# Performance work log

Measured on AMD Instinct MI355X. Metric: run time of the kernel, lower is better.

Reference implementation:

```python
import jax, jax.numpy as jnp
import numpy as np

NODE_DIM = 128
EDGE_DIM = 128
N_NODES = 10000
N_EDGES = 640000


def setup_inputs() -> dict:
    key = jax.random.key(0)
    ks = jax.random.split(key, 11)
    x = jax.random.normal(ks[0], (N_NODES, NODE_DIM), dtype=jnp.float32)
    edge_index = jax.random.randint(ks[1], (2, N_EDGES), 0, N_NODES, dtype=jnp.int32)
    edge_attr = jax.random.normal(ks[2], (N_EDGES, EDGE_DIM), dtype=jnp.float32)

    def lin(k, fan_in, fan_out):
        kw, kb = jax.random.split(k)
        bound = 1.0 / np.sqrt(fan_in)
        W = jax.random.uniform(kw, (fan_in, fan_out), minval=-bound, maxval=bound, dtype=jnp.float32)
        b = jax.random.uniform(kb, (fan_out,), minval=-bound, maxval=bound, dtype=jnp.float32)
        return W, b

    # node_update: Linear(node+edge -> node), Softplus, Linear(node -> node)
    nW1, nb1 = lin(ks[3], NODE_DIM + EDGE_DIM, NODE_DIM)
    nW2, nb2 = lin(ks[4], NODE_DIM, NODE_DIM)
    # edge_update_net: Linear(2*node+edge -> edge), Softplus, Linear(edge -> edge)
    eW1, eb1 = lin(ks[5], 2 * NODE_DIM + EDGE_DIM, EDGE_DIM)
    eW2, eb2 = lin(ks[6], EDGE_DIM, EDGE_DIM)

    return {
        "x": x, "edge_index": edge_index, "edge_attr": edge_attr,
        "nW1": nW1, "nb1": nb1, "nW2": nW2, "nb2": nb2,
        "eW1": eW1, "eb1": eb1, "eW2": eW2, "eb2": eb2,
    }


def reference(x, edge_index, edge_attr, nW1, nb1, nW2, nb2, eW1, eb1, eW2, eb2):
    row, col = edge_index[0], edge_index[1]
    x_row = x[row]              # [E, node_dim]
    x_col = x[col]              # [E, node_dim]

    # edge update MLP
    edge_input = jnp.concatenate([x_row, x_col, edge_attr], axis=1)  # [E, 2n+e]
    h = jax.nn.softplus(edge_input @ eW1 + eb1)
    edge_attr_new = h @ eW2 + eb2                                     # [E, edge_dim]

    # node message MLP
    msg_in = jnp.concatenate([x_row, edge_attr_new], axis=1)          # [E, n+e]
    m = jax.nn.softplus(msg_in @ nW1 + nb1)
    messages = m @ nW2 + nb2                                          # [E, node_dim]

    # scatter_add messages into destination nodes (col)
    x_new = jax.ops.segment_sum(messages, col, num_segments=x.shape[0])
    return (x_new, edge_attr_new)
```

## Files before the change

### kernel.cpp

```cpp
#include <hip/hip_runtime.h>
#include <cstdint>

#define N_NODES   10000
#define N_EDGES   640000
#define NODE_OUT  (N_NODES * 128)

typedef __bf16 bf16;
typedef bf16  bf16x8 __attribute__((ext_vector_type(8)));
typedef float f32x4  __attribute__((ext_vector_type(4)));

#define EW1T_OFF 0
#define EW2T_OFF 49152
#define NW1T_OFF 65536
#define NW2T_OFF 98304

__global__ void transpose_weights(const float* __restrict__ eW1, const float* __restrict__ eW2,
                                  const float* __restrict__ nW1, const float* __restrict__ nW2,
                                  bf16* __restrict__ wt) {
  int gid = blockIdx.x * 256 + threadIdx.x;
  const float* src; bf16* dst; int K, off;
  if (gid < 49152)      { src = eW1; dst = wt + EW1T_OFF; K = 384; off = gid; }
  else if (gid < 65536) { src = eW2; dst = wt + EW2T_OFF; K = 128; off = gid - 49152; }
  else if (gid < 98304) { src = nW1; dst = wt + NW1T_OFF; K = 256; off = gid - 65536; }
  else                  { src = nW2; dst = wt + NW2T_OFF; K = 128; off = gid - 98304; }
  int k = off >> 7, n = off & 127;
  dst[n * K + k] = (bf16)src[off];
}

__device__ __forceinline__ float softplus_f(float v) {
  return v > 20.f ? v : __logf(1.f + __expf(v));
}

__device__ __forceinline__ bf16x8 load_cvt8(const float* __restrict__ src) {
  float4 f0 = *(const float4*)src;
  float4 f1 = *(const float4*)(src + 4);
  bf16x8 h;
  h[0] = (bf16)f0.x; h[1] = (bf16)f0.y; h[2] = (bf16)f0.z; h[3] = (bf16)f0.w;
  h[4] = (bf16)f1.x; h[5] = (bf16)f1.y; h[6] = (bf16)f1.z; h[7] = (bf16)f1.w;
  return h;
}

__global__ void __launch_bounds__(256, 2)
edge_mlp(const float* __restrict__ x, const int* __restrict__ eidx,
         const float* __restrict__ edge_attr,
         const float* __restrict__ eb1, const float* __restrict__ eb2,
         const bf16* __restrict__ wt,
         float* __restrict__ edge_out)
{
  __shared__ bf16 sA[64 * 384];
  __shared__ bf16 sC[64 * 128];

  const int tid  = threadIdx.x;
  const int wave = tid >> 6, lane = tid & 63;
  const int ln15 = lane & 15, lq = lane >> 4;
  const int n0 = wave * 32;
  const int sw = ln15 & 7;

  bf16x8 w1[12][2], w2[4][2];
  #pragma unroll
  for (int c = 0; c < 12; ++c)
    #pragma unroll
    for (int t = 0; t < 2; ++t)
      w1[c][t] = *(const bf16x8*)&wt[EW1T_OFF + (n0 + t * 16 + ln15) * 384 + c * 32 + lq * 8];
  #pragma unroll
  for (int c = 0; c < 4; ++c)
    #pragma unroll
    for (int t = 0; t < 2; ++t)
      w2[c][t] = *(const bf16x8*)&wt[EW2T_OFF + (n0 + t * 16 + ln15) * 128 + c * 32 + lq * 8];
  float b1[2], b2[2];
  #pragma unroll
  for (int t = 0; t < 2; ++t) {
    b1[t] = eb1[n0 + t * 16 + ln15];
    b2[t] = eb2[n0 + t * 16 + ln15];
  }

  for (int tile = blockIdx.x; tile < N_EDGES / 64; tile += gridDim.x) {
    const int e0 = tile * 64;

    #pragma unroll
    for (int it = 0; it < 12; ++it) {
      int j  = it * 256 + tid;
      int region = j >> 10;
      int jj = j & 1023;
      int e  = jj >> 4, pl = jj & 15;
      int lp = pl ^ (e & 7);
      const float* src;
      if (region == 0)      src = x + (size_t)eidx[e0 + e] * 128 + lp * 8;
      else if (region == 1) src = x + (size_t)eidx[N_EDGES + e0 + e] * 128 + lp * 8;
      else                  src = edge_attr + (size_t)(e0 + e) * 128 + lp * 8;
      *(bf16x8*)&sA[e * 384 + ((region << 4) + pl) * 8] = load_cvt8(src);
    }
    __syncthreads();

    f32x4 acc[4][2];
    #pragma unroll
    for (int mf = 0; mf < 4; ++mf)
      #pragma unroll
      for (int t = 0; t < 2; ++t)
        acc[mf][t] = f32x4{0.f, 0.f, 0.f, 0.f};
    #pragma unroll
    for (int c = 0; c < 12; ++c) {
      bf16x8 a[4];
      #pragma unroll
      for (int mf = 0; mf < 4; ++mf)
        a[mf] = *(const bf16x8*)&sA[(mf * 16 + ln15) * 384 + ((((c << 2) + lq) ^ sw) << 3)];
      #pragma unroll
      for (int mf = 0; mf < 4; ++mf)
        #pragma unroll
        for (int t = 0; t < 2; ++t)
          acc[mf][t] = __builtin_amdgcn_mfma_f32_16x16x32_bf16(a[mf], w1[c][t], acc[mf][t], 0, 0, 0);
    }

    #pragma unroll
    for (int mf = 0; mf < 4; ++mf)
      #pragma unroll
      for (int t = 0; t < 2; ++t)
        #pragma unroll
        for (int r = 0; r < 4; ++r) {
          float v = softplus_f(acc[mf][t][r] + b1[t]);
          int row = mf * 16 + lq * 4 + r;
          int col = n0 + t * 16 + ln15;
          int ls  = col >> 3;
          sC[row * 128 + ((ls ^ (row & 7)) << 3) + (col & 7)] = (bf16)v;
        }
    __syncthreads();

    #pragma unroll
    for (int mf = 0; mf < 4; ++mf)
      #pragma unroll
      for (int t = 0; t < 2; ++t)
        acc[mf][t] = f32x4{0.f, 0.f, 0.f, 0.f};
    #pragma unroll
    for (int c = 0; c < 4; ++c) {
      bf16x8 a[4];
      #pragma unroll
      for (int mf = 0; mf < 4; ++mf)
        a[mf] = *(const bf16x8*)&sC[(mf * 16 + ln15) * 128 + ((((c << 2) + lq) ^ sw) << 3)];
      #pragma unroll
      for (int mf = 0; mf < 4; ++mf)
        #pragma unroll
        for (int t = 0; t < 2; ++t)
          acc[mf][t] = __builtin_amdgcn_mfma_f32_16x16x32_bf16(a[mf], w2[c][t], acc[mf][t], 0, 0, 0);
    }
    #pragma unroll
    for (int mf = 0; mf < 4; ++mf)
      #pragma unroll
      for (int t = 0; t < 2; ++t)
        #pragma unroll
        for (int r = 0; r < 4; ++r) {
          int row = mf * 16 + lq * 4 + r;
          int col = n0 + t * 16 + ln15;
          edge_out[(size_t)(e0 + row) * 128 + col] = acc[mf][t][r] + b2[t];
        }
  }
}

__global__ void __launch_bounds__(256, 2)
node_mlp(const float* __restrict__ x, const int* __restrict__ eidx,
         const float* __restrict__ edge_new,
         const float* __restrict__ nb1, const float* __restrict__ nb2,
         const bf16* __restrict__ wt,
         float* __restrict__ node_out)
{
  __shared__ bf16 sA[64 * 384];

  const int tid  = threadIdx.x;
  const int wave = tid >> 6, lane = tid & 63;
  const int ln15 = lane & 15, lq = lane >> 4;
  const int n0 = wave * 32;
  const int sw = ln15 & 7;

  bf16x8 w3[8][2], w4[4][2];
  #pragma unroll
  for (int c = 0; c < 8; ++c)
    #pragma unroll
    for (int t = 0; t < 2; ++t)
      w3[c][t] = *(const bf16x8*)&wt[NW1T_OFF + (n0 + t * 16 + ln15) * 256 + c * 32 + lq * 8];
  #pragma unroll
  for (int c = 0; c < 4; ++c)
    #pragma unroll
    for (int t = 0; t < 2; ++t)
      w4[c][t] = *(const bf16x8*)&wt[NW2T_OFF + (n0 + t * 16 + ln15) * 128 + c * 32 + lq * 8];
  float b3[2], b4[2];
  #pragma unroll
  for (int t = 0; t < 2; ++t) {
    b3[t] = nb1[n0 + t * 16 + ln15];
    b4[t] = nb2[n0 + t * 16 + ln15];
  }

  for (int tile = blockIdx.x; tile < N_EDGES / 64; tile += gridDim.x) {
    const int e0 = tile * 64;

    #pragma unroll
    for (int it = 0; it < 8; ++it) {
      int j  = it * 256 + tid;
      int region = j >> 10;
      int jj = j & 1023;
      int e  = jj >> 4, pl = jj & 15;
      int lp = pl ^ (e & 7);
      const float* src = (region == 0)
          ? x + (size_t)eidx[e0 + e] * 128 + lp * 8
          : edge_new + (size_t)(e0 + e) * 128 + lp * 8;
      *(bf16x8*)&sA[e * 384 + ((region << 4) + pl) * 8] = load_cvt8(src);
    }
    __syncthreads();

    f32x4 acc[4][2];
    #pragma unroll
    for (int mf = 0; mf < 4; ++mf)
      #pragma unroll
      for (int t = 0; t < 2; ++t)
        acc[mf][t] = f32x4{0.f, 0.f, 0.f, 0.f};
    #pragma unroll
    for (int c = 0; c < 8; ++c) {
      bf16x8 a[4];
      #pragma unroll
      for (int mf = 0; mf < 4; ++mf)
        a[mf] = *(const bf16x8*)&sA[(mf * 16 + ln15) * 384 + ((((c << 2) + lq) ^ sw) << 3)];
      #pragma unroll
      for (int mf = 0; mf < 4; ++mf)
        #pragma unroll
        for (int t = 0; t < 2; ++t)
          acc[mf][t] = __builtin_amdgcn_mfma_f32_16x16x32_bf16(a[mf], w3[c][t], acc[mf][t], 0, 0, 0);
    }

    #pragma unroll
    for (int mf = 0; mf < 4; ++mf)
      #pragma unroll
      for (int t = 0; t < 2; ++t)
        #pragma unroll
        for (int r = 0; r < 4; ++r) {
          float v = softplus_f(acc[mf][t][r] + b3[t]);
          int row = mf * 16 + lq * 4 + r;
          int col = n0 + t * 16 + ln15;
          int ls  = 32 + (col >> 3);
          sA[row * 384 + ((ls ^ (row & 7)) << 3) + (col & 7)] = (bf16)v;
        }
    __syncthreads();

    #pragma unroll
    for (int mf = 0; mf < 4; ++mf)
      #pragma unroll
      for (int t = 0; t < 2; ++t)
        acc[mf][t] = f32x4{0.f, 0.f, 0.f, 0.f};
    #pragma unroll
    for (int c = 0; c < 4; ++c) {
      bf16x8 a[4];
      #pragma unroll
      for (int mf = 0; mf < 4; ++mf)
        a[mf] = *(const bf16x8*)&sA[(mf * 16 + ln15) * 384 + (((32 + (c << 2) + lq) ^ sw) << 3)];
      #pragma unroll
      for (int mf = 0; mf < 4; ++mf)
        #pragma unroll
        for (int t = 0; t < 2; ++t)
          acc[mf][t] = __builtin_amdgcn_mfma_f32_16x16x32_bf16(a[mf], w4[c][t], acc[mf][t], 0, 0, 0);
    }
    #pragma unroll
    for (int mf = 0; mf < 4; ++mf) {
      int nodes[4];
      #pragma unroll
      for (int r = 0; r < 4; ++r)
        nodes[r] = eidx[N_EDGES + e0 + mf * 16 + lq * 4 + r];
      #pragma unroll
      for (int t = 0; t < 2; ++t) {
        int col = n0 + t * 16 + ln15;
        #pragma unroll
        for (int r = 0; r < 4; ++r) {
          float v = acc[mf][t][r] + b4[t];
          unsafeAtomicAdd(&node_out[(size_t)nodes[r] * 128 + col], v);
        }
      }
    }
  }
}

extern "C" void kernel_launch(void* const* d_in, const int* in_sizes, int n_in,
                              void* d_out, int out_size, void* d_ws, size_t ws_size,
                              hipStream_t stream) {
  const float* x    = (const float*)d_in[0];
  const int*   eidx = (const int*)d_in[1];
  const float* ea   = (const float*)d_in[2];
  const float* nW1  = (const float*)d_in[3];
  const float* nb1  = (const float*)d_in[4];
  const float* nW2  = (const float*)d_in[5];
  const float* nb2  = (const float*)d_in[6];
  const float* eW1  = (const float*)d_in[7];
  const float* eb1  = (const float*)d_in[8];
  const float* eW2  = (const float*)d_in[9];
  const float* eb2  = (const float*)d_in[10];

  bf16*  wt        = (bf16*)d_ws;
  float* out_nodes = (float*)d_out;
  float* out_edges = out_nodes + NODE_OUT;

  hipMemsetAsync(out_nodes, 0, NODE_OUT * sizeof(float), stream);
  transpose_weights<<<448, 256, 0, stream>>>(eW1, eW2, nW1, nW2, wt);
  edge_mlp<<<512, 256, 0, stream>>>(x, eidx, ea, eb1, eb2, wt, out_edges);
  node_mlp<<<512, 256, 0, stream>>>(x, eidx, out_edges, nb1, nb2, wt, out_nodes);
}
```

Baseline: 992.5 us.

## Prefetch next edge tile into registers, halve tile size, and pre-convert x to bf16

Edge and node MLP kernels now use 32-edge tiles and software-pipeline the gathers: the next tile's x rows and edge features are loaded into registers while the current tile is computed. When workspace allows, x is converted to bf16 once so gathers read half the bytes. The smaller tile roughly halves LDS use, which may raise occupancy, but it also halves MFMA work per barrier and adds register pressure from the prefetch buffers.

New measurement: 839.2 us. 1.18x faster.

```diff
diff --git a/kernel.cpp b/kernel.cpp
--- a/kernel.cpp
+++ b/kernel.cpp
@@ -13,6 +13,8 @@
 #define EW2T_OFF 49152
 #define NW1T_OFF 65536
 #define NW2T_OFF 98304
+#define XB_OFF   114688
+#define WS_NEED_BYTES (229376 + 2560000)
 
 __global__ void transpose_weights(const float* __restrict__ eW1, const float* __restrict__ eW2,
                                   const float* __restrict__ nW1, const float* __restrict__ nW2,
@@ -31,24 +33,33 @@
   return v > 20.f ? v : __logf(1.f + __expf(v));
 }
 
-__device__ __forceinline__ bf16x8 load_cvt8(const float* __restrict__ src) {
-  float4 f0 = *(const float4*)src;
-  float4 f1 = *(const float4*)(src + 4);
+__device__ __forceinline__ bf16x8 cvt8(float4 f0, float4 f1) {
   bf16x8 h;
   h[0] = (bf16)f0.x; h[1] = (bf16)f0.y; h[2] = (bf16)f0.z; h[3] = (bf16)f0.w;
   h[4] = (bf16)f1.x; h[5] = (bf16)f1.y; h[6] = (bf16)f1.z; h[7] = (bf16)f1.w;
   return h;
 }
 
+__device__ __forceinline__ bf16x8 load_cvt8(const float* __restrict__ src) {
+  float4 f0 = *(const float4*)src;
+  float4 f1 = *(const float4*)(src + 4);
+  return cvt8(f0, f1);
+}
+
+__global__ void convert_x(const float* __restrict__ x, bf16* __restrict__ xb) {
+  int i = (blockIdx.x * 256 + threadIdx.x) * 8;
+  *(bf16x8*)&xb[i] = load_cvt8(x + i);
+}
+
+template<bool XB>
 __global__ void __launch_bounds__(256, 2)
-edge_mlp(const float* __restrict__ x, const int* __restrict__ eidx,
-         const float* __restrict__ edge_attr,
+edge_mlp(const float* __restrict__ x, const bf16* __restrict__ xb,
+         const int* __restrict__ eidx, const float* __restrict__ edge_attr,
          const float* __restrict__ eb1, const float* __restrict__ eb2,
-         const bf16* __restrict__ wt,
-         float* __restrict__ edge_out)
+         const bf16* __restrict__ wt, float* __restrict__ edge_out)
 {
-  __shared__ bf16 sA[64 * 384];
-  __shared__ bf16 sC[64 * 128];
+  __shared__ bf16 sA[32 * 384];
+  __shared__ bf16 sC[32 * 128];
 
   const int tid  = threadIdx.x;
   const int wave = tid >> 6, lane = tid & 63;
@@ -74,45 +85,104 @@
     b2[t] = eb2[n0 + t * 16 + ln15];
   }
 
-  for (int tile = blockIdx.x; tile < N_EDGES / 64; tile += gridDim.x) {
-    const int e0 = tile * 64;
-
-    #pragma unroll
-    for (int it = 0; it < 12; ++it) {
-      int j  = it * 256 + tid;
-      int region = j >> 10;
-      int jj = j & 1023;
-      int e  = jj >> 4, pl = jj & 15;
-      int lp = pl ^ (e & 7);
-      const float* src;
-      if (region == 0)      src = x + (size_t)eidx[e0 + e] * 128 + lp * 8;
-      else if (region == 1) src = x + (size_t)eidx[N_EDGES + e0 + e] * 128 + lp * 8;
-      else                  src = edge_attr + (size_t)(e0 + e) * 128 + lp * 8;
-      *(bf16x8*)&sA[e * 384 + ((region << 4) + pl) * 8] = load_cvt8(src);
+  const int eA = tid >> 4, eB = eA + 16;
+  const int pl = tid & 15, lp = pl ^ (eA & 7);
+
+  uint4  hx0, hx1, hc0, hc1;
+  float4 px0[2], px1[2], pc0[2], pc1[2];
+  float4 pa0[2], pa1[2];
+
+  const int NT = N_EDGES / 32;
+
+  {
+    const int e0 = blockIdx.x * 32;
+    int riA = eidx[e0 + eA], riB = eidx[e0 + eB];
+    int ciA = eidx[N_EDGES + e0 + eA], ciB = eidx[N_EDGES + e0 + eB];
+    if constexpr (XB) {
+      hx0 = *(const uint4*)&xb[(size_t)riA * 128 + lp * 8];
+      hx1 = *(const uint4*)&xb[(size_t)riB * 128 + lp * 8];
+      hc0 = *(const uint4*)&xb[(size_t)ciA * 128 + lp * 8];
+      hc1 = *(const uint4*)&xb[(size_t)ciB * 128 + lp * 8];
+    } else {
+      px0[0] = *(const float4*)(x + (size_t)riA * 128 + lp * 8);
+      px0[1] = *(const float4*)(x + (size_t)riA * 128 + lp * 8 + 4);
+      px1[0] = *(const float4*)(x + (size_t)riB * 128 + lp * 8);
+      px1[1] = *(const float4*)(x + (size_t)riB * 128 + lp * 8 + 4);
+      pc0[0] = *(const float4*)(x + (size_t)ciA * 128 + lp * 8);
+      pc0[1] = *(const float4*)(x + (size_t)ciA * 128 + lp * 8 + 4);
+      pc1[0] = *(const float4*)(x + (size_t)ciB * 128 + lp * 8);
+      pc1[1] = *(const float4*)(x + (size_t)ciB * 128 + lp * 8 + 4);
+    }
+    pa0[0] = *(const float4*)(edge_attr + (size_t)(e0 + eA) * 128 + lp * 8);
+    pa0[1] = *(const float4*)(edge_attr + (size_t)(e0 + eA) * 128 + lp * 8 + 4);
+    pa1[0] = *(const float4*)(edge_attr + (size_t)(e0 + eB) * 128 + lp * 8);
+    pa1[1] = *(const float4*)(edge_attr + (size_t)(e0 + eB) * 128 + lp * 8 + 4);
+  }
+
+  for (int tile = blockIdx.x; tile < NT; tile += gridDim.x) {
+    const int e0 = tile * 32;
+
+    if constexpr (XB) {
+      *(uint4*)&sA[eA * 384 + (0 * 16 + pl) * 8] = hx0;
+      *(uint4*)&sA[eB * 384 + (0 * 16 + pl) * 8] = hx1;
+      *(uint4*)&sA[eA * 384 + (1 * 16 + pl) * 8] = hc0;
+      *(uint4*)&sA[eB * 384 + (1 * 16 + pl) * 8] = hc1;
+    } else {
+      *(bf16x8*)&sA[eA * 384 + (0 * 16 + pl) * 8] = cvt8(px0[0], px0[1]);
+      *(bf16x8*)&sA[eB * 384 + (0 * 16 + pl) * 8] = cvt8(px1[0], px1[1]);
+      *(bf16x8*)&sA[eA * 384 + (1 * 16 + pl) * 8] = cvt8(pc0[0], pc0[1]);
+      *(bf16x8*)&sA[eB * 384 + (1 * 16 + pl) * 8] = cvt8(pc1[0], pc1[1]);
+    }
+    *(bf16x8*)&sA[eA * 384 + (2 * 16 + pl) * 8] = cvt8(pa0[0], pa0[1]);
+    *(bf16x8*)&sA[eB * 384 + (2 * 16 + pl) * 8] = cvt8(pa1[0], pa1[1]);
+
+    const int tn = tile + gridDim.x;
+    if (tn < NT) {
+      const int en = tn * 32;
+      int riA = eidx[en + eA], riB = eidx[en + eB];
+      int ciA = eidx[N_EDGES + en + eA], ciB = eidx[N_EDGES + en + eB];
+      if constexpr (XB) {
+        hx0 = *(const uint4*)&xb[(size_t)riA * 128 + lp * 8];
+        hx1 = *(const uint4*)&xb[(size_t)riB * 128 + lp * 8];
+        hc0 = *(const uint4*)&xb[(size_t)ciA * 128 + lp * 8];
+        hc1 = *(const uint4*)&xb[(size_t)ciB * 128 + lp * 8];
+      } else {
+        px0[0] = *(const float4*)(x + (size_t)riA * 128 + lp * 8);
+        px0[1] = *(const float4*)(x + (size_t)riA * 128 + lp * 8 + 4);
+        px1[0] = *(const float4*)(x + (size_t)riB * 128 + lp * 8);
+        px1[1] = *(const float4*)(x + (size_t)riB * 128 + lp * 8 + 4);
+        pc0[0] = *(const float4*)(x + (size_t)ciA * 128 + lp * 8);
+        pc0[1] = *(const float4*)(x + (size_t)ciA * 128 + lp * 8 + 4);
+        pc1[0] = *(const float4*)(x + (size_t)ciB * 128 + lp * 8);
+        pc1[1] = *(const float4*)(x + (size_t)ciB * 128 + lp * 8 + 4);
+      }
+      pa0[0] = *(const float4*)(edge_attr + (size_t)(en + eA) * 128 + lp * 8);
+      pa0[1] = *(const float4*)(edge_attr + (size_t)(en + eA) * 128 + lp * 8 + 4);
+      pa1[0] = *(const float4*)(edge_attr + (size_t)(en + eB) * 128 + lp * 8);
+      pa1[1] = *(const float4*)(edge_attr + (size_t)(en + eB) * 128 + lp * 8 + 4);
     }
     __syncthreads();
 
-    f32x4 acc[4][2];
-    #pragma unroll
-    for (int mf = 0; mf < 4; ++mf)
+    f32x4 acc[2][2];
+    #pragma unroll
+    for (int mf = 0; mf < 2; ++mf)
       #pragma unroll
       for (int t = 0; t < 2; ++t)
         acc[mf][t] = f32x4{0.f, 0.f, 0.f, 0.f};
     #pragma unroll
     for (int c = 0; c < 12; ++c) {
-      bf16x8 a[4];
-      #pragma unroll
-      for (int mf = 0; mf < 4; ++mf)
-        a[mf] = *(const bf16x8*)&sA[(mf * 16 + ln15) * 384 + ((((c << 2) + lq) ^ sw) << 3)];
-      #pragma unroll
-      for (int mf = 0; mf < 4; ++mf)
-        #pragma unroll
-        for (int t = 0; t < 2; ++t)
-          acc[mf][t] = __builtin_amdgcn_mfma_f32_16x16x32_bf16(a[mf], w1[c][t], acc[mf][t], 0, 0, 0);
-    }
-
-    #pragma unroll
-    for (int mf = 0; mf < 4; ++mf)
+      int s = (((c * 4 + lq) ^ sw) << 3);
+      bf16x8 a0 = *(const bf16x8*)&sA[ln15 * 384 + s];
+      bf16x8 a1 = *(const bf16x8*)&sA[(16 + ln15) * 384 + s];
+      #pragma unroll
+      for (int t = 0; t < 2; ++t) {
+        acc[0][t] = __builtin_amdgcn_mfma_f32_16x16x32_bf16(a0, w1[c][t], acc[0][t], 0, 0, 0);
+        acc[1][t] = __builtin_amdgcn_mfma_f32_16x16x32_bf16(a1, w1[c][t], acc[1][t], 0, 0, 0);
+      }
+    }
+
+    #pragma unroll
+    for (int mf = 0; mf < 2; ++mf)
       #pragma unroll
       for (int t = 0; t < 2; ++t)
         #pragma unroll
@@ -120,49 +190,47 @@
           float v = softplus_f(acc[mf][t][r] + b1[t]);
           int row = mf * 16 + lq * 4 + r;
           int col = n0 + t * 16 + ln15;
-          int ls  = col >> 3;
-          sC[row * 128 + ((ls ^ (row & 7)) << 3) + (col & 7)] = (bf16)v;
+          sC[row * 128 + ((((col >> 3) ^ (row & 7))) << 3) + (col & 7)] = (bf16)v;
         }
     __syncthreads();
 
-    #pragma unroll
-    for (int mf = 0; mf < 4; ++mf)
-      #pragma unroll
-      for (int t = 0; t < 2; ++t)
-        acc[mf][t] = f32x4{0.f, 0.f, 0.f, 0.f};
+    f32x4 d[2][2];
+    #pragma unroll
+    for (int mf = 0; mf < 2; ++mf)
+      #pragma unroll
+      for (int t = 0; t < 2; ++t)
+        d[mf][t] = f32x4{0.f, 0.f, 0.f, 0.f};
     #pragma unroll
     for (int c = 0; c < 4; ++c) {
-      bf16x8 a[4];
-      #pragma unroll
-      for (int mf = 0; mf < 4; ++mf)
-        a[mf] = *(const bf16x8*)&sC[(mf * 16 + ln15) * 128 + ((((c << 2) + lq) ^ sw) << 3)];
-      #pragma unroll
-      for (int mf = 0; mf < 4; ++mf)
-        #pragma unroll
-        for (int t = 0; t < 2; ++t)
-          acc[mf][t] = __builtin_amdgcn_mfma_f32_16x16x32_bf16(a[mf], w2[c][t], acc[mf][t], 0, 0, 0);
-    }
-    #pragma unroll
-    for (int mf = 0; mf < 4; ++mf)
+      int s = (((c * 4 + lq) ^ sw) << 3);
+      bf16x8 a0 = *(const bf16x8*)&sC[ln15 * 128 + s];
+      bf16x8 a1 = *(const bf16x8*)&sC[(16 + ln15) * 128 + s];
+      #pragma unroll
+      for (int t = 0; t < 2; ++t) {
+        d[0][t] = __builtin_amdgcn_mfma_f32_16x16x32_bf16(a0, w2[c][t], d[0][t], 0, 0, 0);
+        d[1][t] = __builtin_amdgcn_mfma_f32_16x16x32_bf16(a1, w2[c][t], d[1][t], 0, 0, 0);
+      }
+    }
+    #pragma unroll
+    for (int mf = 0; mf < 2; ++mf)
       #pragma unroll
       for (int t = 0; t < 2; ++t)
         #pragma unroll
         for (int r = 0; r < 4; ++r) {
           int row = mf * 16 + lq * 4 + r;
-          int col = n0 + t * 16 + ln15;
-          edge_out[(size_t)(e0 + row) * 128 + col] = acc[mf][t][r] + b2[t];
+          edge_out[(size_t)(e0 + row) * 128 + n0 + t * 16 + ln15] = d[mf][t][r] + b2[t];
         }
   }
 }
 
+template<bool XB>
 __global__ void __launch_bounds__(256, 2)
-node_mlp(const float* __restrict__ x, const int* __restrict__ eidx,
-         const float* __restrict__ edge_new,
+node_mlp(const float* __restrict__ x, const bf16* __restrict__ xb,
+         const int* __restrict__ eidx, const float* __restrict__ edge_new,
          const float* __restrict__ nb1, const float* __restrict__ nb2,
-         const bf16* __restrict__ wt,
-         float* __restrict__ node_out)
+         const bf16* __restrict__ wt, float* __restrict__ node_out)
 {
-  __shared__ bf16 sA[64 * 384];
+  __shared__ bf16 sA[32 * 384];
 
   const int tid  = threadIdx.x;
   const int wave = tid >> 6, lane = tid & 63;
@@ -188,44 +256,86 @@
     b4[t] = nb2[n0 + t * 16 + ln15];
   }
 
-  for (int tile = blockIdx.x; tile < N_EDGES / 64; tile += gridDim.x) {
-    const int e0 = tile * 64;
-
-    #pragma unroll
-    for (int it = 0; it < 8; ++it) {
-      int j  = it * 256 + tid;
-      int region = j >> 10;
-      int jj = j & 1023;
-      int e  = jj >> 4, pl = jj & 15;
-      int lp = pl ^ (e & 7);
-      const float* src = (region == 0)
-          ? x + (size_t)eidx[e0 + e] * 128 + lp * 8
-          : edge_new + (size_t)(e0 + e) * 128 + lp * 8;
-      *(bf16x8*)&sA[e * 384 + ((region << 4) + pl) * 8] = load_cvt8(src);
+  const int eA = tid >> 4, eB = eA + 16;
+  const int pl = tid & 15, lp = pl ^ (eA & 7);
+
+  uint4  hx0, hx1;
+  float4 px0[2], px1[2];
+  float4 pe0[2], pe1[2];
+
+  const int NT = N_EDGES / 32;
+
+  {
+    const int e0 = blockIdx.x * 32;
+    int riA = eidx[e0 + eA], riB = eidx[e0 + eB];
+    if constexpr (XB) {
+      hx0 = *(const uint4*)&xb[(size_t)riA * 128 + lp * 8];
+      hx1 = *(const uint4*)&xb[(size_t)riB * 128 + lp * 8];
+    } else {
+      px0[0] = *(const float4*)(x + (size_t)riA * 128 + lp * 8);
+      px0[1] = *(const float4*)(x + (size_t)riA * 128 + lp * 8 + 4);
+      px1[0] = *(const float4*)(x + (size_t)riB * 128 + lp * 8);
+      px1[1] = *(const float4*)(x + (size_t)riB * 128 + lp * 8 + 4);
+    }
+    pe0[0] = *(const float4*)(edge_new + (size_t)(e0 + eA) * 128 + lp * 8);
+    pe0[1] = *(const float4*)(edge_new + (size_t)(e0 + eA) * 128 + lp * 8 + 4);
+    pe1[0] = *(const float4*)(edge_new + (size_t)(e0 + eB) * 128 + lp * 8);
+    pe1[1] = *(const float4*)(edge_new + (size_t)(e0 + eB) * 128 + lp * 8 + 4);
+  }
+
+  for (int tile = blockIdx.x; tile < NT; tile += gridDim.x) {
+    const int e0 = tile * 32;
+
+    if constexpr (XB) {
+      *(uint4*)&sA[eA * 384 + (0 * 16 + pl) * 8] = hx0;
+      *(uint4*)&sA[eB * 384 + (0 * 16 + pl) * 8] = hx1;
+    } else {
+      *(bf16x8*)&sA[eA * 384 + (0 * 16 + pl) * 8] = cvt8(px0[0], px0[1]);
+      *(bf16x8*)&sA[eB * 384 + (0 * 16 + pl) * 8] = cvt8(px1[0], px1[1]);
+    }
+    *(bf16x8*)&sA[eA * 384 + (1 * 16 + pl) * 8] = cvt8(pe0[0], pe0[1]);
+    *(bf16x8*)&sA[eB * 384 + (1 * 16 + pl) * 8] = cvt8(pe1[0], pe1[1]);
+
+    const int tn = tile + gridDim.x;
+    if (tn < NT) {
+      const int en = tn * 32;
+      int riA = eidx[en + eA], riB = eidx[en + eB];
+      if constexpr (XB) {
+        hx0 = *(const uint4*)&xb[(size_t)riA * 128 + lp * 8];
+        hx1 = *(const uint4*)&xb[(size_t)riB * 128 + lp * 8];
+      } else {
+        px0[0] = *(const float4*)(x + (size_t)riA * 128 + lp * 8);
+        px0[1] = *(const float4*)(x + (size_t)riA * 128 + lp * 8 + 4);
+        px1[0] = *(const float4*)(x + (size_t)riB * 128 + lp * 8);
+        px1[1] = *(const float4*)(x + (size_t)riB * 128 + lp * 8 + 4);
+      }
+      pe0[0] = *(const float4*)(edge_new + (size_t)(en + eA) * 128 + lp * 8);
+      pe0[1] = *(const float4*)(edge_new + (size_t)(en + eA) * 128 + lp * 8 + 4);
+      pe1[0] = *(const float4*)(edge_new + (size_t)(en + eB) * 128 + lp * 8);
+      pe1[1] = *(const float4*)(edge_new + (size_t)(en + eB) * 128 + lp * 8 + 4);
     }
     __syncthreads();
 
-    f32x4 acc[4][2];
-    #pragma unroll
-    for (int mf = 0; mf < 4; ++mf)
+    f32x4 acc[2][2];
+    #pragma unroll
+    for (int mf = 0; mf < 2; ++mf)
       #pragma unroll
       for (int t = 0; t < 2; ++t)
         acc[mf][t] = f32x4{0.f, 0.f, 0.f, 0.f};
     #pragma unroll
     for (int c = 0; c < 8; ++c) {
-      bf16x8 a[4];
-      #pragma unroll
-      for (int mf = 0; mf < 4; ++mf)
-        a[mf] = *(const bf16x8*)&sA[(mf * 16 + ln15) * 384 + ((((c << 2) + lq) ^ sw) << 3)];
-      #pragma unroll
-      for (int mf = 0; mf < 4; ++mf)
-        #pragma unroll
-        for (int t = 0; t < 2; ++t)
-          acc[mf][t] = __builtin_amdgcn_mfma_f32_16x16x32_bf16(a[mf], w3[c][t], acc[mf][t], 0, 0, 0);
-    }
-
-    #pragma unroll
-    for (int mf = 0; mf < 4; ++mf)
+      int s = (((c * 4 + lq) ^ sw) << 3);
+      bf16x8 a0 = *(const bf16x8*)&sA[ln15 * 384 + s];
+      bf16x8 a1 = *(const bf16x8*)&sA[(16 + ln15) * 384 + s];
+      #pragma unroll
+      for (int t = 0; t < 2; ++t) {
+        acc[0][t] = __builtin_amdgcn_mfma_f32_16x16x32_bf16(a0, w3[c][t], acc[0][t], 0, 0, 0);
+        acc[1][t] = __builtin_amdgcn_mfma_f32_16x16x32_bf16(a1, w3[c][t], acc[1][t], 0, 0, 0);
+      }
+    }
+
+    #pragma unroll
+    for (int mf = 0; mf < 2; ++mf)
       #pragma unroll
       for (int t = 0; t < 2; ++t)
         #pragma unroll
@@ -238,36 +348,34 @@
         }
     __syncthreads();
 
-    #pragma unroll
-    for (int mf = 0; mf < 4; ++mf)
-      #pragma unroll
-      for (int t = 0; t < 2; ++t)
-        acc[mf][t] = f32x4{0.f, 0.f, 0.f, 0.f};
+    f32x4 d[2][2];
+    #pragma unroll
+    for (int mf = 0; mf < 2; ++mf)
+      #pragma unroll
+      for (int t = 0; t < 2; ++t)
+        d[mf][t] = f32x4{0.f, 0.f, 0.f, 0.f};
     #pragma unroll
     for (int c = 0; c < 4; ++c) {
-      bf16x8 a[4];
-      #pragma unroll
-      for (int mf = 0; mf < 4; ++mf)
-        a[mf] = *(const bf16x8*)&sA[(mf * 16 + ln15) * 384 + (((32 + (c << 2) + lq) ^ sw) << 3)];
-      #pragma unroll
-      for (int mf = 0; mf < 4; ++mf)
-        #pragma unroll
-        for (int t = 0; t < 2; ++t)
-          acc[mf][t] = __builtin_amdgcn_mfma_f32_16x16x32_bf16(a[mf], w4[c][t], acc[mf][t], 0, 0, 0);
-    }
-    #pragma unroll
-    for (int mf = 0; mf < 4; ++mf) {
-      int nodes[4];
-      #pragma unroll
-      for (int r = 0; r < 4; ++r)
-        nodes[r] = eidx[N_EDGES + e0 + mf * 16 + lq * 4 + r];
+      int s = (((32 + c * 4 + lq) ^ sw) << 3);
+      bf16x8 a0 = *(const bf16x8*)&sA[ln15 * 384 + s];
+      bf16x8 a1 = *(const bf16x8*)&sA[(16 + ln15) * 384 + s];
+      #pragma unroll
+      for (int t = 0; t < 2; ++t) {
+        d[0][t] = __builtin_amdgcn_mfma_f32_16x16x32_bf16(a0, w4[c][t], d[0][t], 0, 0, 0);
+        d[1][t] = __builtin_amdgcn_mfma_f32_16x16x32_bf16(a1, w4[c][t], d[1][t], 0, 0, 0);
+      }
+    }
+    #pragma unroll
+    for (int mf = 0; mf < 2; ++mf) {
+      int4 q = *(const int4*)&eidx[N_EDGES + e0 + mf * 16 + lq * 4];
+      int nid[4] = {q.x, q.y, q.z, q.w};
       #pragma unroll
       for (int t = 0; t < 2; ++t) {
         int col = n0 + t * 16 + ln15;
         #pragma unroll
         for (int r = 0; r < 4; ++r) {
-          float v = acc[mf][t][r] + b4[t];
-          unsafeAtomicAdd(&node_out[(size_t)nodes[r] * 128 + col], v);
+          float v = d[mf][t][r] + b4[t];
+          unsafeAtomicAdd(&node_out[(size_t)nid[r] * 128 + col], v);
         }
       }
     }
@@ -295,6 +403,15 @@
 
   hipMemsetAsync(out_nodes, 0, NODE_OUT * sizeof(float), stream);
   transpose_weights<<<448, 256, 0, stream>>>(eW1, eW2, nW1, nW2, wt);
-  edge_mlp<<<512, 256, 0, stream>>>(x, eidx, ea, eb1, eb2, wt, out_edges);
-  node_mlp<<<512, 256, 0, stream>>>(x, eidx, out_edges, nb1, nb2, wt, out_nodes);
-}
+
+  const bool use_xb = ws_size >= (size_t)WS_NEED_BYTES;
+  bf16* xb = wt + XB_OFF;
+  if (use_xb) {
+    convert_x<<<625, 256, 0, stream>>>(x, xb);
+    edge_mlp<true><<<512, 256, 0, stream>>>(x, xb, eidx, ea, eb1, eb2, wt, out_edges);
+    node_mlp<true><<<512, 256, 0, stream>>>(x, xb, eidx, out_edges, nb1, nb2, wt, out_nodes);
+  } else {
+    edge_mlp<false><<<512, 256, 0, stream>>>(x, nullptr, eidx, ea, eb1, eb2, wt, out_edges);
+    node_mlp<false><<<512, 256, 0, stream>>>(x, nullptr, eidx, out_edges, nb1, nb2, wt, out_nodes);
+  }
+}
```
